# Performance work log

Measured on AMD Instinct MI355X. Metric: run time of the kernel, lower is better.

## Reference

```python
import jax, jax.numpy as jnp
import numpy as np

D_MODEL = 192
D_INNER = 384   # expand=2
D_STATE = 16
D_CONV = 4
DT_RANK = 12    # ceil(192/16)
DEPTH = 4
STRIDE = 4
N_PATCH = 400   # 1600 // 4
NCLS = 1000
BATCH = 32
EPS = 1e-5


def setup_inputs() -> dict:
    key = jax.random.key(0)
    ks = iter(jax.random.split(key, 64))
    nrm = lambda shp, s=0.02: jax.random.normal(next(ks), shp, jnp.float32) * s
    inp = {}
    inp["imgs"] = jax.random.normal(next(ks), (BATCH, 1, 40, 40), jnp.float32)
    # StrideEmbed: conv1d(kernel=stride=4) == per-patch linear on [B,400,4]
    inp["patch_w"] = nrm((STRIDE, D_MODEL))
    inp["patch_b"] = jnp.zeros((D_MODEL,), jnp.float32)
    inp["cls_token"] = nrm((1, 1, D_MODEL))
    inp["pos_embed"] = nrm((1, N_PATCH + 1, D_MODEL))
    # per-block Mamba params, stacked on a leading depth axis
    inp["norm_ws"] = jnp.ones((DEPTH, D_MODEL), jnp.float32)
    inp["in_proj_ws"] = nrm((DEPTH, D_MODEL, 2 * D_INNER))
    inp["conv_ws"] = nrm((DEPTH, D_INNER, D_CONV), 0.2)
    inp["conv_bs"] = jnp.zeros((DEPTH, D_INNER), jnp.float32)
    inp["x_proj_ws"] = nrm((DEPTH, D_INNER, DT_RANK + 2 * D_STATE))
    inp["dt_proj_ws"] = nrm((DEPTH, DT_RANK, D_INNER), 0.1)
    # dt bias ~ inverse-softplus of small positive dt
    inp["dt_proj_bs"] = jnp.log(jnp.expm1(jnp.full((DEPTH, D_INNER), 0.01, jnp.float32)))
    inp["A_logs"] = jnp.log(jnp.broadcast_to(
        jnp.arange(1, D_STATE + 1, dtype=jnp.float32), (DEPTH, D_INNER, D_STATE)))
    inp["Ds"] = jnp.ones((DEPTH, D_INNER), jnp.float32)
    inp["out_proj_ws"] = nrm((DEPTH, D_INNER, D_MODEL))
    inp["norm_f_w"] = jnp.ones((D_MODEL,), jnp.float32)
    inp["head_w"] = nrm((D_MODEL, NCLS))
    inp["head_b"] = jnp.zeros((NCLS,), jnp.float32)
    return inp


def rmsnorm(x, w):
    return x * jax.lax.rsqrt(jnp.mean(x * x, axis=-1, keepdims=True) + EPS) * w


def mamba_mixer(x, in_w, conv_w, conv_b, xp_w, dt_w, dt_b, A_log, Dp, out_w):
    # x: [B, L, D_MODEL]
    B, L, _ = x.shape
    xz = x @ in_w                         # [B, L, 2*d_inner]
    u, z = jnp.split(xz, 2, axis=-1)
    # causal depthwise conv1d (kernel 4), truncated to L, then SiLU
    upad = jnp.pad(u, ((0, 0), (D_CONV - 1, 0), (0, 0)))
    uc = sum(upad[:, k:k + L, :] * conv_w[:, k] for k in range(D_CONV)) + conv_b
    uc = jax.nn.silu(uc)
    # input-dependent dt, B, C
    dbl = uc @ xp_w                       # [B, L, dt_rank + 2*d_state]
    dt = dbl[..., :DT_RANK]
    Bm = dbl[..., DT_RANK:DT_RANK + D_STATE]
    Cm = dbl[..., DT_RANK + D_STATE:]
    delta = jax.nn.softplus(dt @ dt_w + dt_b)           # [B, L, d_inner]
    A = -jnp.exp(A_log)                                  # [d_inner, d_state]
    dA = jnp.exp(delta[..., None] * A)                   # [B, L, d_inner, d_state]
    dBu = (delta * uc)[..., None] * Bm[:, :, None, :]    # [B, L, d_inner, d_state]

    def step(h, t):
        da, dbu, c = t
        h = da * h + dbu                                 # [B, d_inner, d_state]
        y = jnp.einsum('bds,bs->bd', h, c)
        return h, y

    h0 = jnp.zeros((B, D_INNER, D_STATE), x.dtype)
    _, ys = jax.lax.scan(step, h0, (jnp.moveaxis(dA, 1, 0),
                                    jnp.moveaxis(dBu, 1, 0),
                                    jnp.moveaxis(Cm, 1, 0)))
    y = jnp.moveaxis(ys, 0, 1) + uc * Dp                 # [B, L, d_inner]
    return (y * jax.nn.silu(z)) @ out_w


def reference(imgs, patch_w, patch_b, cls_token, pos_embed, norm_ws, in_proj_ws,
              conv_ws, conv_bs, x_proj_ws, dt_proj_ws, dt_proj_bs, A_logs, Ds,
              out_proj_ws, norm_f_w, head_w, head_b):
    B = imgs.shape[0]
    seq = imgs.reshape(B, N_PATCH, STRIDE)               # [B, 400, 4] (in_chans=1)
    x = seq @ patch_w + patch_b + pos_embed[:, :-1, :]   # patch embed + pos (cls pos is last)
    cls = cls_token + pos_embed[:, -1:, :]
    x = jnp.concatenate([x, jnp.broadcast_to(cls, (B, 1, D_MODEL))], axis=1)  # cls appended at end
    residual = None
    for i in range(DEPTH):
        residual = x if residual is None else x + residual  # fused add-norm, prenorm
        h = rmsnorm(residual, norm_ws[i])
        x = mamba_mixer(h, in_proj_ws[i], conv_ws[i], conv_bs[i], x_proj_ws[i],
                        dt_proj_ws[i], dt_proj_bs[i], A_logs[i], Ds[i], out_proj_ws[i])
    x = rmsnorm(x + residual, norm_f_w)                   # final fused add-norm, prenorm=False
    return x[:, -1, :] @ head_w + head_b                  # head on cls (last) token
```

## Files before the change

### kernel.cpp

```cpp
#include <hip/hip_runtime.h>
#include <hip/hip_bf16.h>
#include <hip/hip_fp16.h>

using bf16 = __hip_bfloat16;
typedef short short8 __attribute__((ext_vector_type(8)));
typedef float floatx4 __attribute__((ext_vector_type(4)));

#define LSEQ 401
#define NTOK 12832
#define NTOKP 12928
#define DM 192
#define DI 384
#define NB 32
#define NCH 13
#define CHT 32
#define SLAB ((long)NTOKP * 44)

#define O_IMGS   0
#define O_PW     51200
#define O_PB     51968
#define O_CLS    52160
#define O_POS    52352
#define O_NORMW  129344
#define O_INW    130112
#define O_CONVW  719936
#define O_CONVB  726080
#define O_XPW    727616
#define O_DTW    795200
#define O_DTB    813632
#define O_ALOG   815168
#define O_DS     839744
#define O_OUTW   841280
#define O_NORMF  1136192
#define O_HEADW  1136384
#define O_HEADB  1328384
#define WTOT     1329408

#define BO_INWT  0
#define BO_XPWT  589824
#define BO_OUTWT 688128
#define BFTOT_F  491520

__constant__ int g_sz[18] = {51200, 768, 192, 192, 76992, 768, 589824, 6144, 1536,
                             67584, 18432, 1536, 24576, 1536, 294912, 192, 192000, 1000};
__constant__ int g_off[18] = {O_IMGS, O_PW, O_PB, O_CLS, O_POS, O_NORMW, O_INW, O_CONVW,
                              O_CONVB, O_XPW, O_DTW, O_DTB, O_ALOG, O_DS, O_OUTW,
                              O_NORMF, O_HEADW, O_HEADB};

struct SrcPtrs { const void* p[18]; };

static __device__ __forceinline__ int probe_flag(const unsigned short* probe) {
    unsigned short u0 = probe[0];
    if (u0 == 0x3F80u) return 0;
    if (u0 == 0x3C00u) return 2;
    return 1;
}
static __device__ __forceinline__ float load_src(int flag, const void* p, long i) {
    if (flag == 0) return __bfloat162float(((const bf16*)p)[i]);
    if (flag == 2) return __half2float(((const __half*)p)[i]);
    return ((const float*)p)[i];
}
static __device__ __forceinline__ unsigned short f2b(float f) {
    bf16 h = __float2bfloat16(f);
    return *reinterpret_cast<unsigned short*>(&h);
}
static __device__ __forceinline__ float b2f_us(unsigned short us) {
    unsigned int ui = (unsigned int)us << 16;
    return __uint_as_float(ui);
}

__global__ void convert_kernel(SrcPtrs sp, const unsigned short* __restrict__ probe,
                               float* __restrict__ dst) {
    int flag = probe_flag(probe);
    int which = blockIdx.y;
    int n = g_sz[which];
    const void* src = sp.p[which];
    float* d = dst + g_off[which];
    for (int i = blockIdx.x * blockDim.x + threadIdx.x; i < n; i += gridDim.x * blockDim.x)
        d[i] = load_src(flag, src, i);
}

__global__ void prep_wt_kernel(SrcPtrs sp, const unsigned short* __restrict__ probe,
                               unsigned short* __restrict__ bfw) {
    int flag = probe_flag(probe);
    int which = blockIdx.y, layer = blockIdx.z;
    int i = blockIdx.x * 256 + threadIdx.x;
    if (which == 0) {
        if (i >= 768 * 192) return;
        int n = i / 192, k = i % 192;
        float v = load_src(flag, sp.p[6], (long)layer * 147456 + (long)k * 768 + n);
        bfw[BO_INWT + (long)layer * 147456 + i] = f2b(v);
    } else if (which == 1) {
        if (i >= 64 * 384) return;
        int n = i / 384, k = i % 384;
        float v = (n < 44) ? load_src(flag, sp.p[9], (long)layer * 16896 + (long)k * 44 + n) : 0.f;
        bfw[BO_XPWT + (long)layer * 24576 + i] = f2b(v);
    } else {
        if (i >= 192 * 384) return;
        int n = i / 384, k = i % 384;
        float v = load_src(flag, sp.p[14], (long)layer * 73728 + (long)k * 192 + n);
        bfw[BO_OUTWT + (long)layer * 73728 + i] = f2b(v);
    }
}

__global__ __launch_bounds__(192) void embed_kernel(const float* __restrict__ W, float* __restrict__ x) {
    const float* imgs = W + O_IMGS;
    const float* pw   = W + O_PW;
    const float* pb   = W + O_PB;
    const float* cls  = W + O_CLS;
    const float* pos  = W + O_POS;
    int tok = blockIdx.x;
    int b = tok / LSEQ, t = tok % LSEQ;
    int c = threadIdx.x;
    float v;
    if (t < 400) {
        float s0 = imgs[b * 1600 + t * 4 + 0];
        float s1 = imgs[b * 1600 + t * 4 + 1];
        float s2 = imgs[b * 1600 + t * 4 + 2];
        float s3 = imgs[b * 1600 + t * 4 + 3];
        v = s0 * pw[0 * DM + c] + s1 * pw[1 * DM + c] +
            s2 * pw[2 * DM + c] + s3 * pw[3 * DM + c] + pb[c] + pos[t * DM + c];
    } else {
        v = cls[c] + pos[400 * DM + c];
    }
    x[(long)tok * DM + c] = v;
}

__global__ __launch_bounds__(256) void resnorm_kernel(
    const float* __restrict__ x, float* __restrict__ res, unsigned short* __restrict__ hbf,
    const float* __restrict__ w, int first) {
    int wv = threadIdx.x >> 6, lane = threadIdx.x & 63;
    long tok = (long)blockIdx.x * 4 + wv;
    long base = tok * DM + lane * 4;
    float4 v = make_float4(0.f, 0.f, 0.f, 0.f);
    bool real = (tok < NTOK);
    if (real && lane < 48) {
        v = *(const float4*)(x + base);
        if (!first) {
            float4 r = *(const float4*)(res + base);
            v.x += r.x; v.y += r.y; v.z += r.z; v.w += r.w;
        }
        *(float4*)(res + base) = v;
    }
    float ss = v.x * v.x + v.y * v.y + v.z * v.z + v.w * v.w;
#pragma unroll
    for (int o = 1; o < 64; o <<= 1) ss += __shfl_xor(ss, o, 64);
    float inv = rsqrtf(ss * (1.f / DM) + 1e-5f);
    if (lane < 48) {
        if (real) {
            float4 w4 = *(const float4*)(w + lane * 4);
            ushort4 h;
            h.x = f2b(v.x * inv * w4.x); h.y = f2b(v.y * inv * w4.y);
            h.z = f2b(v.z * inv * w4.z); h.w = f2b(v.w * inv * w4.w);
            *(ushort4*)(hbf + base) = h;
        } else if (tok < NTOKP) {
            ushort4 h; h.x = h.y = h.z = h.w = 0;
            *(ushort4*)(hbf + base) = h;
        }
    }
}

template <int OUTBF>
__global__ __launch_bounds__(256) void gemm_mfma(
    const unsigned short* __restrict__ A, const unsigned short* __restrict__ Wt,
    void* __restrict__ Cv, int K, int N, int NC, int sa, int sw,
    long zA, long zW, long zC) {
    __shared__ unsigned short sA[128][72];
    __shared__ unsigned short sW[64][72];
    A += (long)blockIdx.z * zA;
    Wt += (long)blockIdx.z * zW;
    int tid = threadIdx.x;
    int w = tid >> 6, lane = tid & 63;
    int q = lane >> 4, m = lane & 15;
    long tok0 = (long)blockIdx.x * 128;
    int n0 = blockIdx.y * 64;
    floatx4 acc[2][4] = {};
    for (int k0 = 0; k0 < K; k0 += 64) {
#pragma unroll
        for (int p = 0; p < 4; ++p) {
            int idx = tid + p * 256;
            int r = idx >> 3, c8 = (idx & 7) * 8;
            *(short8*)&sA[r][c8] = *(const short8*)(A + (tok0 + r) * sa + k0 + c8);
        }
#pragma unroll
        for (int p = 0; p < 2; ++p) {
            int idx = tid + p * 256;
            int r = idx >> 3, c8 = (idx & 7) * 8;
            *(short8*)&sW[r][c8] = *(const short8*)(Wt + (long)(n0 + r) * sw + k0 + c8);
        }
        __syncthreads();
#pragma unroll
        for (int q2 = 0; q2 < 64; q2 += 32) {
#pragma unroll
            for (int tf = 0; tf < 2; ++tf) {
                short8 bfr = *(const short8*)&sA[w * 32 + tf * 16 + m][q2 + q * 8];
#pragma unroll
                for (int nt = 0; nt < 4; ++nt) {
                    short8 afr = *(const short8*)&sW[nt * 16 + m][q2 + q * 8];
                    acc[tf][nt] = __builtin_amdgcn_mfma_f32_16x16x32_bf16(afr, bfr, acc[tf][nt], 0, 0, 0);
                }
            }
        }
        __syncthreads();
    }
#pragma unroll
    for (int tf = 0; tf < 2; ++tf) {
        long tok = tok0 + w * 32 + tf * 16 + m;
#pragma unroll
        for (int nt = 0; nt < 4; ++nt) {
            int ch = n0 + nt * 16 + q * 4;
            if (OUTBF) {
                unsigned short* dst = (unsigned short*)Cv + (long)blockIdx.z * zC + tok * NC + ch;
                ushort4 h4;
                h4.x = f2b(acc[tf][nt][0]); h4.y = f2b(acc[tf][nt][1]);
                h4.z = f2b(acc[tf][nt][2]); h4.w = f2b(acc[tf][nt][3]);
                *(ushort4*)dst = h4;
            } else {
                float* dst = (float*)Cv + (long)blockIdx.z * zC + tok * NC + ch;
                if (ch + 3 < N) {
                    *(float4*)dst = make_float4(acc[tf][nt][0], acc[tf][nt][1], acc[tf][nt][2], acc[tf][nt][3]);
                } else {
#pragma unroll
                    for (int r = 0; r < 4; ++r)
                        if (ch + r < N) dst[r] = acc[tf][nt][r];
                }
            }
        }
    }
}

__global__ __launch_bounds__(384) void conv_silu_kernel(
    const unsigned short* __restrict__ xzb, const float* __restrict__ cw,
    const float* __restrict__ cb, unsigned short* __restrict__ ucb) {
    int b = blockIdx.y;
    int t0 = blockIdx.x * 8;
    int d = threadIdx.x;
    float w0 = cw[d * 4 + 0], w1 = cw[d * 4 + 1], w2 = cw[d * 4 + 2], w3 = cw[d * 4 + 3];
    float bias = cb[d];
    long tb = (long)b * LSEQ;
    float uv[11];
#pragma unroll
    for (int j = 0; j < 11; ++j) {
        int t = t0 - 3 + j;
        uv[j] = (t >= 0 && t < LSEQ) ? b2f_us(xzb[(tb + t) * 768 + d]) : 0.f;
    }
#pragma unroll
    for (int j = 0; j < 8; ++j) {
        int t = t0 + j;
        if (t < LSEQ) {
            float acc = bias + w0 * uv[j] + w1 * uv[j + 1] + w2 * uv[j + 2] + w3 * uv[j + 3];
            float sv = acc / (1.f + __expf(-acc));
            ucb[(tb + t) * DI + d] = f2b(sv);
        }
    }
}

__global__ __launch_bounds__(256) void scan_sum_kernel(
    const float* __restrict__ dblP, const unsigned short* __restrict__ ucb,
    const float* __restrict__ dtw, const float* __restrict__ dtb,
    const float* __restrict__ Alog, float* __restrict__ deltaBuf,
    float* __restrict__ Aprod, float* __restrict__ Hend) {
    int ch = blockIdx.x, b = blockIdx.y;
    int tid = threadIdx.x;
    int shalf = tid & 1;
    int d = blockIdx.z * 128 + (tid >> 1);
    int t0 = ch * CHT;
    long tokb = (long)b * LSEQ + t0;
    int tmax = min(CHT, LSEQ - t0);
    bool last = (ch == NCH - 1);
    __shared__ float sdt[CHT][12];
    __shared__ float sB[CHT][16];
    for (int i = tid; i < tmax * 12; i += 256) {
        int r = i / 12, k = i % 12;
        long o = (tokb + r) * 44 + k;
        sdt[r][k] = dblP[o] + dblP[o + SLAB] + dblP[o + 2 * SLAB];
    }
    if (!last) {
        for (int i = tid; i < CHT * 16; i += 256) {
            int r = i >> 4, s = i & 15;
            long o = (tokb + r) * 44 + 12 + s;
            sB[r][s] = dblP[o] + dblP[o + SLAB] + dblP[o + 2 * SLAB];
        }
    }
    float dtwr[12];
#pragma unroll
    for (int k = 0; k < 12; ++k) dtwr[k] = dtw[k * DI + d];
    float bias = dtb[d];
    float a[8];
#pragma unroll
    for (int s = 0; s < 8; ++s) a[s] = -__expf(Alog[d * 16 + shalf * 8 + s]);
    float h[8] = {};
    float sumd = 0.f;
    __syncthreads();
    float u0 = b2f_us(ucb[tokb * DI + d]);
    float u1 = b2f_us(ucb[(tokb + min(1, tmax - 1)) * DI + d]);
#pragma unroll 2
    for (int t = 0; t < tmax; ++t) {
        int tp = min(t + 2, tmax - 1);
        float u2 = b2f_us(ucb[(tokb + tp) * DI + d]);
        float acc = bias;
#pragma unroll
        for (int k = 0; k < 12; ++k) acc = fmaf(sdt[t][k], dtwr[k], acc);
        float delta = (acc > 20.f) ? acc : __logf(1.f + __expf(acc));
        if (shalf == 0) deltaBuf[(tokb + t) * DI + d] = delta;
        if (!last) {
            float du = delta * u0;
            sumd += delta;
            float Bv[8];
            *(float4*)&Bv[0] = *(const float4*)&sB[t][shalf * 8];
            *(float4*)&Bv[4] = *(const float4*)&sB[t][shalf * 8 + 4];
#pragma unroll
            for (int s = 0; s < 8; ++s) {
                float da = __expf(delta * a[s]);
                h[s] = fmaf(da, h[s], du * Bv[s]);
            }
        }
        u0 = u1; u1 = u2;
    }
    if (!last) {
        long idx = (((long)b * NCH + ch) * DI + d) * 16 + shalf * 8;
        float ap[8], he[8];
#pragma unroll
        for (int s = 0; s < 8; ++s) { ap[s] = __expf(a[s] * sumd); he[s] = h[s]; }
        *(float4*)(Aprod + idx) = *(float4*)&ap[0];
        *(float4*)(Aprod + idx + 4) = *(float4*)&ap[4];
        *(float4*)(Hend + idx) = *(float4*)&he[0];
        *(float4*)(Hend + idx + 4) = *(float4*)&he[4];
    }
}

__global__ __launch_bounds__(256) void scan_combine_kernel(
    const float* __restrict__ Ap, const float* __restrict__ He, float* __restrict__ hinit) {
    long gid = (long)blockIdx.x * 256 + threadIdx.x;
    int b = (int)(gid / 6144);
    int r = (int)(gid % 6144);
    float carry = 0.f;
#pragma unroll
    for (int j = 0; j < NCH; ++j) {
        long idx = ((long)b * NCH + j) * 6144 + r;
        hinit[idx] = carry;
        if (j < NCH - 1) carry = fmaf(Ap[idx], carry, He[idx]);
    }
}

__global__ __launch_bounds__(256) void scan_main_kernel(
    const float* __restrict__ deltaBuf, const unsigned short* __restrict__ ucb,
    const unsigned short* __restrict__ xzb, const float* __restrict__ Alog,
    const float* __restrict__ Dvec, const float* __restrict__ hinit,
    const float* __restrict__ dblP, unsigned short* __restrict__ ybf) {
    int ch = blockIdx.x, b = blockIdx.y;
    int tid = threadIdx.x;
    int shalf = tid & 1;
    int d = blockIdx.z * 128 + (tid >> 1);
    int t0 = ch * CHT;
    long tokb = (long)b * LSEQ + t0;
    int tmax = min(CHT, LSEQ - t0);
    __shared__ float sB[CHT][16], sC[CHT][16];
    for (int i = tid; i < CHT * 16; i += 256) {
        int r = i >> 4, s = i & 15;
        if (r < tmax) {
            long o = (tokb + r) * 44 + 12 + s;
            sB[r][s] = dblP[o] + dblP[o + SLAB] + dblP[o + 2 * SLAB];
            sC[r][s] = dblP[o + 16] + dblP[o + 16 + SLAB] + dblP[o + 16 + 2 * SLAB];
        } else {
            sB[r][s] = 0.f; sC[r][s] = 0.f;
        }
    }
    float a[8];
#pragma unroll
    for (int s = 0; s < 8; ++s) a[s] = -__expf(Alog[d * 16 + shalf * 8 + s]);
    float h[8];
    long hidx = (((long)b * NCH + ch) * DI + d) * 16 + shalf * 8;
    *(float4*)&h[0] = *(const float4*)(hinit + hidx);
    *(float4*)&h[4] = *(const float4*)(hinit + hidx + 4);
    float Dp = Dvec[d];
    __syncthreads();
    int t1i = min(1, tmax - 1);
    float d0 = deltaBuf[tokb * DI + d];
    float u0 = b2f_us(ucb[tokb * DI + d]);
    float z0 = b2f_us(xzb[tokb * 768 + DI + d]);
    float d1 = deltaBuf[(tokb + t1i) * DI + d];
    float u1 = b2f_us(ucb[(tokb + t1i) * DI + d]);
    float z1 = b2f_us(xzb[(tokb + t1i) * 768 + DI + d]);
#pragma unroll 2
    for (int t = 0; t < tmax; ++t) {
        int tp = min(t + 2, tmax - 1);
        float d2 = deltaBuf[(tokb + tp) * DI + d];
        float u2 = b2f_us(ucb[(tokb + tp) * DI + d]);
        float z2 = b2f_us(xzb[(tokb + tp) * 768 + DI + d]);
        float Bv[8], Cv[8];
        *(float4*)&Bv[0] = *(const float4*)&sB[t][shalf * 8];
        *(float4*)&Bv[4] = *(const float4*)&sB[t][shalf * 8 + 4];
        *(float4*)&Cv[0] = *(const float4*)&sC[t][shalf * 8];
        *(float4*)&Cv[4] = *(const float4*)&sC[t][shalf * 8 + 4];
        float du = d0 * u0;
        float y0 = 0.f, y1 = 0.f, y2 = 0.f, y3 = 0.f;
#pragma unroll
        for (int s = 0; s < 8; s += 4) {
            float da0 = __expf(d0 * a[s]);
            float da1 = __expf(d0 * a[s + 1]);
            float da2 = __expf(d0 * a[s + 2]);
            float da3 = __expf(d0 * a[s + 3]);
            h[s]     = fmaf(da0, h[s],     du * Bv[s]);
            h[s + 1] = fmaf(da1, h[s + 1], du * Bv[s + 1]);
            h[s + 2] = fmaf(da2, h[s + 2], du * Bv[s + 2]);
            h[s + 3] = fmaf(da3, h[s + 3], du * Bv[s + 3]);
            y0 = fmaf(h[s],     Cv[s],     y0);
            y1 = fmaf(h[s + 1], Cv[s + 1], y1);
            y2 = fmaf(h[s + 2], Cv[s + 2], y2);
            y3 = fmaf(h[s + 3], Cv[s + 3], y3);
        }
        float p = (y0 + y1) + (y2 + y3);
        p += __shfl_xor(p, 1, 64);
        if (shalf == 0) {
            float y = fmaf(u0, Dp, p);
            float gz = z0 / (1.f + __expf(-z0));
            ybf[(tokb + t) * DI + d] = f2b(y * gz);
        }
        d0 = d1; u0 = u1; z0 = z1;
        d1 = d2; u1 = u2; z1 = z2;
    }
}

__global__ __launch_bounds__(256) void finalnorm_kernel(
    const float* __restrict__ x, const float* __restrict__ res,
    const float* __restrict__ w, float* __restrict__ v) {
    int b = blockIdx.x;
    int c = threadIdx.x;
    long tok = (long)b * LSEQ + 400;
    __shared__ float sb[256];
    float val = 0.f;
    if (c < DM) val = x[tok * DM + c] + res[tok * DM + c];
    sb[c] = val * val;
    __syncthreads();
    for (int o = 128; o > 0; o >>= 1) {
        if (c < o) sb[c] += sb[c + o];
        __syncthreads();
    }
    float inv = rsqrtf(sb[0] * (1.f / DM) + 1e-5f);
    if (c < DM) v[b * DM + c] = val * inv * w[c];
}

__global__ __launch_bounds__(128) void head_kernel(
    const float* __restrict__ v, const float* __restrict__ hw, const float* __restrict__ hb,
    const unsigned short* __restrict__ probe, void* __restrict__ out) {
    int b = blockIdx.y;
    int n = blockIdx.x * 128 + threadIdx.x;
    __shared__ float vs[DM];
    for (int i = threadIdx.x; i < DM; i += 128) vs[i] = v[b * DM + i];
    __syncthreads();
    if (n < 1000) {
        float acc = hb[n];
#pragma unroll 4
        for (int c = 0; c < DM; ++c) acc = fmaf(vs[c], hw[c * 1000 + n], acc);
        int flag = probe_flag(probe);
        if (flag == 0)      ((bf16*)out)[b * 1000 + n] = (bf16)acc;
        else if (flag == 2) ((__half*)out)[b * 1000 + n] = __float2half(acc);
        else                ((float*)out)[b * 1000 + n] = acc;
    }
}

extern "C" void kernel_launch(void* const* d_in, const int* in_sizes, int n_in,
                              void* d_out, int out_size, void* d_ws, size_t ws_size,
                              hipStream_t stream) {
    float* ws = (float*)d_ws;
    float* Wr = ws;
    unsigned short* bfw = (unsigned short*)(ws + WTOT);
    float* act   = ws + WTOT + BFTOT_F;
    float* resT  = act;
    float* xB    = resT + (long)NTOKP * DM;
    float* dblP  = xB + (long)NTOKP * DM;
    float* Aprod = dblP + 3 * SLAB;
    float* Hend  = Aprod + (long)NB * NCH * 6144;
    float* hinit = Hend + (long)NB * NCH * 6144;
    float* deltaB= hinit + (long)NB * NCH * 6144;
    float* vbuf  = deltaB + (long)NTOKP * DI;
    unsigned short* hbf = (unsigned short*)(vbuf + NB * DM);
    unsigned short* xzb = hbf + (long)NTOKP * DM;
    unsigned short* ucb = xzb + (long)NTOKP * 768;
    unsigned short* ybf = ucb + (long)NTOKP * DI;

    const unsigned short* probe = (const unsigned short*)d_in[5];

    SrcPtrs sp;
    for (int i = 0; i < 18; ++i) sp.p[i] = d_in[i];
    convert_kernel<<<dim3(64, 18), 256, 0, stream>>>(sp, probe, Wr);
    prep_wt_kernel<<<dim3(576, 3, 4), 256, 0, stream>>>(sp, probe, bfw);

    embed_kernel<<<NTOK, 192, 0, stream>>>(Wr, xB);

    for (int i = 0; i < 4; ++i) {
        resnorm_kernel<<<NTOKP / 4, 256, 0, stream>>>(xB, resT, hbf, Wr + O_NORMW + i * DM, i == 0);
        gemm_mfma<1><<<dim3(101, 12), 256, 0, stream>>>(
            hbf, bfw + BO_INWT + (long)i * 147456, xzb, 192, 768, 768, 192, 192, 0, 0, 0);
        conv_silu_kernel<<<dim3(51, NB), 384, 0, stream>>>(
            xzb, Wr + O_CONVW + i * 1536, Wr + O_CONVB + i * DI, ucb);
        gemm_mfma<0><<<dim3(101, 1, 3), 256, 0, stream>>>(
            ucb, bfw + BO_XPWT + (long)i * 24576, dblP, 128, 44, 44, 384, 384, 128, 128, SLAB);
        scan_sum_kernel<<<dim3(NCH, NB, 3), 256, 0, stream>>>(
            dblP, ucb, Wr + O_DTW + i * 4608, Wr + O_DTB + i * DI,
            Wr + O_ALOG + i * 6144, deltaB, Aprod, Hend);
        scan_combine_kernel<<<(NB * 6144) / 256, 256, 0, stream>>>(Aprod, Hend, hinit);
        scan_main_kernel<<<dim3(NCH, NB, 3), 256, 0, stream>>>(
            deltaB, ucb, xzb, Wr + O_ALOG + i * 6144, Wr + O_DS + i * DI,
            hinit, dblP, ybf);
        gemm_mfma<0><<<dim3(101, 3), 256, 0, stream>>>(
            ybf, bfw + BO_OUTWT + (long)i * 73728, xB, 384, 192, 192, 384, 384, 0, 0, 0);
    }

    finalnorm_kernel<<<NB, 256, 0, stream>>>(xB, resT, Wr + O_NORMF, vbuf);
    head_kernel<<<dim3(8, NB), 128, 0, stream>>>(vbuf, Wr + O_HEADW, Wr + O_HEADB, probe, d_out);
}
```

Measured before the change: 639.4 us.

## Fuse residual add and RMSNorm into out-projection GEMM epilogue and embedding

Replaces the separate residual-add/RMSNorm kernel with an epilogue on a new out-projection GEMM that computes all 192 output channels per tile, adds the residual, and writes the next layer's normalized bf16 input. The embedding kernel also performs the first norm, and the final norm is folded into the last layer's epilogue, with the head reading the bf16 normalized cls token. This removes several launches and an fp32 activation buffer round trip. It risks lower GEMM parallelism (fewer, larger blocks) and slight precision loss at the head input.

```diff
diff --git a/kernel.cpp b/kernel.cpp
--- a/kernel.cpp
+++ b/kernel.cpp
@@ -103,15 +103,15 @@
     }
 }
 
-__global__ __launch_bounds__(192) void embed_kernel(const float* __restrict__ W, float* __restrict__ x) {
+__global__ __launch_bounds__(192) void embed_norm_kernel(
+    const float* __restrict__ W, float* __restrict__ res,
+    unsigned short* __restrict__ hbf, const float* __restrict__ nw) {
+    int tok = blockIdx.x;
+    int c = threadIdx.x;
+    if (tok >= NTOK) { hbf[(long)tok * DM + c] = 0; return; }
     const float* imgs = W + O_IMGS;
     const float* pw   = W + O_PW;
-    const float* pb   = W + O_PB;
-    const float* cls  = W + O_CLS;
-    const float* pos  = W + O_POS;
-    int tok = blockIdx.x;
     int b = tok / LSEQ, t = tok % LSEQ;
-    int c = threadIdx.x;
     float v;
     if (t < 400) {
         float s0 = imgs[b * 1600 + t * 4 + 0];
@@ -119,45 +119,20 @@
         float s2 = imgs[b * 1600 + t * 4 + 2];
         float s3 = imgs[b * 1600 + t * 4 + 3];
         v = s0 * pw[0 * DM + c] + s1 * pw[1 * DM + c] +
-            s2 * pw[2 * DM + c] + s3 * pw[3 * DM + c] + pb[c] + pos[t * DM + c];
+            s2 * pw[2 * DM + c] + s3 * pw[3 * DM + c] +
+            W[O_PB + c] + W[O_POS + t * DM + c];
     } else {
-        v = cls[c] + pos[400 * DM + c];
-    }
-    x[(long)tok * DM + c] = v;
-}
-
-__global__ __launch_bounds__(256) void resnorm_kernel(
-    const float* __restrict__ x, float* __restrict__ res, unsigned short* __restrict__ hbf,
-    const float* __restrict__ w, int first) {
-    int wv = threadIdx.x >> 6, lane = threadIdx.x & 63;
-    long tok = (long)blockIdx.x * 4 + wv;
-    long base = tok * DM + lane * 4;
-    float4 v = make_float4(0.f, 0.f, 0.f, 0.f);
-    bool real = (tok < NTOK);
-    if (real && lane < 48) {
-        v = *(const float4*)(x + base);
-        if (!first) {
-            float4 r = *(const float4*)(res + base);
-            v.x += r.x; v.y += r.y; v.z += r.z; v.w += r.w;
-        }
-        *(float4*)(res + base) = v;
-    }
-    float ss = v.x * v.x + v.y * v.y + v.z * v.z + v.w * v.w;
+        v = W[O_CLS + c] + W[O_POS + 400 * DM + c];
+    }
+    res[(long)tok * DM + c] = v;
+    __shared__ float sw[3];
+    float ss = v * v;
 #pragma unroll
     for (int o = 1; o < 64; o <<= 1) ss += __shfl_xor(ss, o, 64);
-    float inv = rsqrtf(ss * (1.f / DM) + 1e-5f);
-    if (lane < 48) {
-        if (real) {
-            float4 w4 = *(const float4*)(w + lane * 4);
-            ushort4 h;
-            h.x = f2b(v.x * inv * w4.x); h.y = f2b(v.y * inv * w4.y);
-            h.z = f2b(v.z * inv * w4.z); h.w = f2b(v.w * inv * w4.w);
-            *(ushort4*)(hbf + base) = h;
-        } else if (tok < NTOKP) {
-            ushort4 h; h.x = h.y = h.z = h.w = 0;
-            *(ushort4*)(hbf + base) = h;
-        }
-    }
+    if ((threadIdx.x & 63) == 0) sw[threadIdx.x >> 6] = ss;
+    __syncthreads();
+    float inv = rsqrtf((sw[0] + sw[1] + sw[2]) * (1.f / DM) + 1e-5f);
+    hbf[(long)tok * DM + c] = f2b(v * inv * nw[c]);
 }
 
 template <int OUTBF>
@@ -226,6 +201,82 @@
                 }
             }
         }
+    }
+}
+
+__global__ __launch_bounds__(256) void outproj_norm_kernel(
+    const unsigned short* __restrict__ ybf, const unsigned short* __restrict__ Wt,
+    float* __restrict__ res, unsigned short* __restrict__ hbf,
+    const float* __restrict__ nw) {
+    __shared__ unsigned short sA[64][72];
+    __shared__ unsigned short sW[192][72];
+    __shared__ float swn[192];
+    int tid = threadIdx.x;
+    int w = tid >> 6, lane = tid & 63;
+    int q = lane >> 4, m = lane & 15;
+    long tok0 = (long)blockIdx.x * 64;
+    if (tid < 192) swn[tid] = nw[tid];
+    floatx4 acc[12] = {};
+    for (int k0 = 0; k0 < 384; k0 += 64) {
+#pragma unroll
+        for (int p = 0; p < 2; ++p) {
+            int idx = tid + p * 256;
+            int r = idx >> 3, c8 = (idx & 7) * 8;
+            *(short8*)&sA[r][c8] = *(const short8*)(ybf + (tok0 + r) * DI + k0 + c8);
+        }
+#pragma unroll
+        for (int p = 0; p < 6; ++p) {
+            int idx = tid + p * 256;
+            int r = idx >> 3, c8 = (idx & 7) * 8;
+            *(short8*)&sW[r][c8] = *(const short8*)(Wt + (long)r * DI + k0 + c8);
+        }
+        __syncthreads();
+#pragma unroll
+        for (int q2 = 0; q2 < 64; q2 += 32) {
+            short8 bfr = *(const short8*)&sA[w * 16 + m][q2 + q * 8];
+#pragma unroll
+            for (int nt = 0; nt < 12; ++nt) {
+                short8 afr = *(const short8*)&sW[nt * 16 + m][q2 + q * 8];
+                acc[nt] = __builtin_amdgcn_mfma_f32_16x16x32_bf16(afr, bfr, acc[nt], 0, 0, 0);
+            }
+        }
+        __syncthreads();
+    }
+    long tok = tok0 + w * 16 + m;
+    bool real = (tok < NTOK);
+    float val[12][4];
+    float ss = 0.f;
+    if (real) {
+#pragma unroll
+        for (int nt = 0; nt < 12; ++nt) {
+            int ch = nt * 16 + q * 4;
+            float4 rv = *(const float4*)(res + tok * DM + ch);
+            val[nt][0] = acc[nt][0] + rv.x;
+            val[nt][1] = acc[nt][1] + rv.y;
+            val[nt][2] = acc[nt][2] + rv.z;
+            val[nt][3] = acc[nt][3] + rv.w;
+            *(float4*)(res + tok * DM + ch) =
+                make_float4(val[nt][0], val[nt][1], val[nt][2], val[nt][3]);
+#pragma unroll
+            for (int r = 0; r < 4; ++r) ss = fmaf(val[nt][r], val[nt][r], ss);
+        }
+    }
+    ss += __shfl_xor(ss, 16, 64);
+    ss += __shfl_xor(ss, 32, 64);
+    float inv = rsqrtf(ss * (1.f / DM) + 1e-5f);
+#pragma unroll
+    for (int nt = 0; nt < 12; ++nt) {
+        int ch = nt * 16 + q * 4;
+        ushort4 h4;
+        if (real) {
+            h4.x = f2b(val[nt][0] * inv * swn[ch + 0]);
+            h4.y = f2b(val[nt][1] * inv * swn[ch + 1]);
+            h4.z = f2b(val[nt][2] * inv * swn[ch + 2]);
+            h4.w = f2b(val[nt][3] * inv * swn[ch + 3]);
+        } else {
+            h4.x = h4.y = h4.z = h4.w = 0;
+        }
+        *(ushort4*)(hbf + tok * DM + ch) = h4;
     }
 }
 
@@ -422,32 +473,15 @@
     }
 }
 
-__global__ __launch_bounds__(256) void finalnorm_kernel(
-    const float* __restrict__ x, const float* __restrict__ res,
-    const float* __restrict__ w, float* __restrict__ v) {
-    int b = blockIdx.x;
-    int c = threadIdx.x;
-    long tok = (long)b * LSEQ + 400;
-    __shared__ float sb[256];
-    float val = 0.f;
-    if (c < DM) val = x[tok * DM + c] + res[tok * DM + c];
-    sb[c] = val * val;
-    __syncthreads();
-    for (int o = 128; o > 0; o >>= 1) {
-        if (c < o) sb[c] += sb[c + o];
-        __syncthreads();
-    }
-    float inv = rsqrtf(sb[0] * (1.f / DM) + 1e-5f);
-    if (c < DM) v[b * DM + c] = val * inv * w[c];
-}
-
 __global__ __launch_bounds__(128) void head_kernel(
-    const float* __restrict__ v, const float* __restrict__ hw, const float* __restrict__ hb,
-    const unsigned short* __restrict__ probe, void* __restrict__ out) {
+    const unsigned short* __restrict__ hbf, const float* __restrict__ hw,
+    const float* __restrict__ hb, const unsigned short* __restrict__ probe,
+    void* __restrict__ out) {
     int b = blockIdx.y;
     int n = blockIdx.x * 128 + threadIdx.x;
     __shared__ float vs[DM];
-    for (int i = threadIdx.x; i < DM; i += 128) vs[i] = v[b * DM + i];
+    long tok = (long)b * LSEQ + 400;
+    for (int i = threadIdx.x; i < DM; i += 128) vs[i] = b2f_us(hbf[tok * DM + i]);
     __syncthreads();
     if (n < 1000) {
         float acc = hb[n];
@@ -468,14 +502,12 @@
     unsigned short* bfw = (unsigned short*)(ws + WTOT);
     float* act   = ws + WTOT + BFTOT_F;
     float* resT  = act;
-    float* xB    = resT + (long)NTOKP * DM;
-    float* dblP  = xB + (long)NTOKP * DM;
+    float* dblP  = resT + (long)NTOKP * DM;
     float* Aprod = dblP + 3 * SLAB;
     float* Hend  = Aprod + (long)NB * NCH * 6144;
     float* hinit = Hend + (long)NB * NCH * 6144;
     float* deltaB= hinit + (long)NB * NCH * 6144;
-    float* vbuf  = deltaB + (long)NTOKP * DI;
-    unsigned short* hbf = (unsigned short*)(vbuf + NB * DM);
+    unsigned short* hbf = (unsigned short*)(deltaB + (long)NTOKP * DI);
     unsigned short* xzb = hbf + (long)NTOKP * DM;
     unsigned short* ucb = xzb + (long)NTOKP * 768;
     unsigned short* ybf = ucb + (long)NTOKP * DI;
@@ -487,10 +519,9 @@
     convert_kernel<<<dim3(64, 18), 256, 0, stream>>>(sp, probe, Wr);
     prep_wt_kernel<<<dim3(576, 3, 4), 256, 0, stream>>>(sp, probe, bfw);
 
-    embed_kernel<<<NTOK, 192, 0, stream>>>(Wr, xB);
+    embed_norm_kernel<<<NTOKP, 192, 0, stream>>>(Wr, resT, hbf, Wr + O_NORMW);
 
     for (int i = 0; i < 4; ++i) {
-        resnorm_kernel<<<NTOKP / 4, 256, 0, stream>>>(xB, resT, hbf, Wr + O_NORMW + i * DM, i == 0);
         gemm_mfma<1><<<dim3(101, 12), 256, 0, stream>>>(
             hbf, bfw + BO_INWT + (long)i * 147456, xzb, 192, 768, 768, 192, 192, 0, 0, 0);
         conv_silu_kernel<<<dim3(51, NB), 384, 0, stream>>>(
@@ -504,10 +535,11 @@
         scan_main_kernel<<<dim3(NCH, NB, 3), 256, 0, stream>>>(
             deltaB, ucb, xzb, Wr + O_ALOG + i * 6144, Wr + O_DS + i * DI,
             hinit, dblP, ybf);
-        gemm_mfma<0><<<dim3(101, 3), 256, 0, stream>>>(
-            ybf, bfw + BO_OUTWT + (long)i * 73728, xB, 384, 192, 192, 384, 384, 0, 0, 0);
-    }
-
-    finalnorm_kernel<<<NB, 256, 0, stream>>>(xB, resT, Wr + O_NORMF, vbuf);
-    head_kernel<<<dim3(8, NB), 128, 0, stream>>>(vbuf, Wr + O_HEADW, Wr + O_HEADB, probe, d_out);
-}
+        const float* nw = (i < 3) ? (Wr + O_NORMW + (i + 1) * DM) : (Wr + O_NORMF);
+        outproj_norm_kernel<<<202, 256, 0, stream>>>(
+            ybf, bfw + BO_OUTWT + (long)i * 73728, resT, hbf, nw);
+    }
+
+    head_kernel<<<dim3(8, NB), 128, 0, stream>>>(
+        hbf, Wr + O_HEADW, Wr + O_HEADB, probe, d_out);
+}
```

Result: no change. 647.5 us (+1.3%).
